# Optimization experiments

Hardware: AMD Instinct MI355X
Metric: run time of the kernel (lower is better)

Reference implementation:

```python
import jax, jax.numpy as jnp
import numpy as np

N_NODES = 50000


def _sage_conv(x, src, dst, W_l, b_l, W_r):
    # PyG SAGEConv (mean aggr): out = lin_l(mean_{j in N(i)} x_j) + lin_r(x_i)
    E = src.shape[0]
    msgs = x[src]                                            # [E, F] gather
    agg = jax.ops.segment_sum(msgs, dst, num_segments=N_NODES)
    deg = jax.ops.segment_sum(jnp.ones((E,), x.dtype), dst, num_segments=N_NODES)
    mean = agg / jnp.maximum(deg, 1.0)[:, None]              # zero-neighbor nodes stay 0
    return mean @ W_l.T + b_l + x @ W_r.T


def setup_inputs() -> dict:
    key = jax.random.key(0)
    k = jax.random.split(key, 8)
    F_in, H1, H2 = 128, 256, 128  # num_features, 2*emb, emb
    E = 800000
    x = jax.random.normal(k[0], (N_NODES, F_in), dtype=jnp.float32)
    edge_index = jax.random.randint(k[1], (2, E), 0, N_NODES, dtype=jnp.int64)
    s1 = 1.0 / np.sqrt(F_in)
    s2 = 1.0 / np.sqrt(H1)
    W1_l = jax.random.uniform(k[2], (H1, F_in), jnp.float32, -s1, s1)
    b1_l = jax.random.uniform(k[3], (H1,), jnp.float32, -s1, s1)
    W1_r = jax.random.uniform(k[4], (H1, F_in), jnp.float32, -s1, s1)
    W2_l = jax.random.uniform(k[5], (H2, H1), jnp.float32, -s2, s2)
    b2_l = jax.random.uniform(k[6], (H2,), jnp.float32, -s2, s2)
    W2_r = jax.random.uniform(k[7], (H2, H1), jnp.float32, -s2, s2)
    return {"x": x, "edge_index": edge_index,
            "W1_l": W1_l, "b1_l": b1_l, "W1_r": W1_r,
            "W2_l": W2_l, "b2_l": b2_l, "W2_r": W2_r}


def reference(x, edge_index, W1_l, b1_l, W1_r, W2_l, b2_l, W2_r):
    src, dst = edge_index[0], edge_index[1]
    h = jax.nn.relu(_sage_conv(x, src, dst, W1_l, b1_l, W1_r))
    # F.dropout(training=self.training): identity at inference
    out = _sage_conv(h, src, dst, W2_l, b2_l, W2_r)
    return out
```

## Files before the change

### kernel.cpp

```cpp
#include <hip/hip_runtime.h>


typedef short bf16x8 __attribute__((ext_vector_type(8)));
typedef float f32x4  __attribute__((ext_vector_type(4)));

__device__ __forceinline__ unsigned f2bf(float f) {
    unsigned u = __float_as_uint(f);
    return (u + 0x7FFFu + ((u >> 16) & 1u)) >> 16;
}
__device__ __forceinline__ unsigned pack2(float a, float b) {
    return f2bf(a) | (f2bf(b) << 16);
}
__device__ __forceinline__ float2 bfunpack(unsigned u) {
    return make_float2(__uint_as_float(u << 16), __uint_as_float(u & 0xffff0000u));
}

__device__ __forceinline__ void scan256(const int* __restrict__ h,
                                        int* __restrict__ out, int tid) {
    if (tid < 64) {
        const int i4 = tid * 4;
        const int v0 = h[i4], v1 = h[i4 + 1], v2 = h[i4 + 2], v3 = h[i4 + 3];
        const int t = v0 + v1 + v2 + v3;
        int x = t;
        #pragma unroll
        for (int dd = 1; dd < 64; dd <<= 1) {
            const int y = __shfl_up(x, dd, 64);
            if (tid >= dd) x += y;
        }
        const int ex = x - t;
        out[i4] = ex; out[i4 + 1] = ex + v0;
        out[i4 + 2] = ex + v0 + v1; out[i4 + 3] = ex + v0 + v1 + v2;
    }
}

__global__ __launch_bounds__(256)
void prep_kernel(const float* __restrict__ x, short* __restrict__ x_bf, long nx,
                 const float* __restrict__ W0, const float* __restrict__ W1,
                 const float* __restrict__ W2, const float* __restrict__ W3,
                 short* __restrict__ wbuf, int wn,
                 const int* __restrict__ dst, int* __restrict__ hist, int E,
                 int nbF, int nbW) {
    const int bx = blockIdx.x, tid = threadIdx.x;
    if (bx < nbF) {
        const long i = ((long)bx * 256 + tid) * 8;
        if (i + 8 <= nx) {
            const float4 a = *(const float4*)(x + i);
            const float4 b = *(const float4*)(x + i + 4);
            *(uint4*)(x_bf + i) = make_uint4(pack2(a.x, a.y), pack2(a.z, a.w),
                                             pack2(b.x, b.y), pack2(b.z, b.w));
        }
    } else if (bx < nbF + nbW) {
        const int rel = bx - nbF;
        const int w = rel >> 7;
        const float* __restrict__ W = (w == 0) ? W0 : (w == 1) ? W1 : (w == 2) ? W2 : W3;
        short* hi = wbuf + (long)(2 * w) * wn;
        short* lo = hi + wn;
        const int i = (rel & 127) * 256 + tid;
        if (i < wn) {
            const float v = W[i];
            const unsigned h = f2bf(v);
            hi[i] = (short)h;
            lo[i] = (short)f2bf(v - __uint_as_float(h << 16));
        }
    } else {
        const int hb = bx - nbF - nbW;
        #pragma unroll
        for (int k = 0; k < 4; ++k) {
            const int i = hb * 1024 + k * 256 + tid;
            if (i < E) atomicAdd(&hist[dst[i]], 1);
        }
    }
}

__global__ __launch_bounds__(256)
void scan_reduce_kernel(const int* __restrict__ hist, int* __restrict__ bsum, int M) {
    const long base = (long)blockIdx.x * 2048 + (long)threadIdx.x * 8;
    int s = 0;
    #pragma unroll
    for (int i = 0; i < 8; ++i) { const long idx = base + i; if (idx < M) s += hist[idx]; }
    #pragma unroll
    for (int d = 32; d; d >>= 1) s += __shfl_down(s, d, 64);
    __shared__ int ws[4];
    const int lane = threadIdx.x & 63, wid = threadIdx.x >> 6;
    if (lane == 0) ws[wid] = s;
    __syncthreads();
    if (threadIdx.x == 0) bsum[blockIdx.x] = ws[0] + ws[1] + ws[2] + ws[3];
}

__global__ void scan_root_kernel(int* __restrict__ bsum, int NB) {
    const int lane = threadIdx.x;
    const int v = (lane < NB) ? bsum[lane] : 0;
    int x = v;
    #pragma unroll
    for (int d = 1; d < 64; d <<= 1) { const int y = __shfl_up(x, d, 64); if (lane >= d) x += y; }
    if (lane < NB) bsum[lane] = x - v;
}

__global__ __launch_bounds__(256)
void scan_apply_kernel(int* __restrict__ hist, const int* __restrict__ bsum,
                       int* __restrict__ offs, int* __restrict__ gcur, int M, int E) {
    const long base = (long)blockIdx.x * 2048 + (long)threadIdx.x * 8;
    int v[8];
    #pragma unroll
    for (int i = 0; i < 8; ++i) { const long idx = base + i; v[i] = (idx < M) ? hist[idx] : 0; }
    int tsum = 0;
    #pragma unroll
    for (int i = 0; i < 8; ++i) { const int t = v[i]; v[i] = tsum; tsum += t; }
    const int lane = threadIdx.x & 63, wid = threadIdx.x >> 6;
    int x = tsum;
    #pragma unroll
    for (int d = 1; d < 64; d <<= 1) { const int y = __shfl_up(x, d, 64); if (lane >= d) x += y; }
    __shared__ int ws[4];
    if (lane == 63) ws[wid] = x;
    __syncthreads();
    int woff = bsum[blockIdx.x];
    if (wid > 0) woff += ws[0];
    if (wid > 1) woff += ws[1];
    if (wid > 2) woff += ws[2];
    const int texcl = woff + x - tsum;
    #pragma unroll
    for (int i = 0; i < 8; ++i) {
        const long idx = base + i;
        if (idx < M) {
            const int o = texcl + v[i];
            offs[idx] = o;
            hist[idx] = 0;
            if ((idx & 255) == 0) gcur[idx >> 8] = o;
        }
    }
    if (blockIdx.x == 0 && threadIdx.x == 0) offs[M] = E;
}

__global__ __launch_bounds__(1024)
void msplit_kernel(const int* __restrict__ src, const int* __restrict__ dst,
                   int* __restrict__ gcur, uint2* __restrict__ staging, int E) {
    __shared__ int hist[256], scanex[256], gb[256];
    __shared__ uint2 pairs[4096];
    const int tid = threadIdx.x;
    const long base = (long)blockIdx.x * 4096;
    const int cnt = min(4096, (int)(E - base));
    if (tid < 256) hist[tid] = 0;
    __syncthreads();
    int d[4], s[4];
    #pragma unroll
    for (int k = 0; k < 4; ++k) {
        const int i = tid + k * 1024;
        if (i < cnt) {
            d[k] = dst[base + i]; s[k] = src[base + i];
            atomicAdd(&hist[d[k] >> 8], 1);
        }
    }
    __syncthreads();
    scan256(hist, scanex, tid);
    __syncthreads();
    if (tid < 256) {
        const int c = hist[tid];
        gb[tid] = c ? atomicAdd(&gcur[tid], c) : 0;
        hist[tid] = scanex[tid];
    }
    __syncthreads();
    #pragma unroll
    for (int k = 0; k < 4; ++k) {
        const int i = tid + k * 1024;
        if (i < cnt) {
            const int b = d[k] >> 8;
            const int pos = atomicAdd(&hist[b], 1);
            pairs[pos] = make_uint2((unsigned)s[k], (unsigned)d[k]);
        }
    }
    __syncthreads();
    #pragma unroll
    for (int k = 0; k < 4; ++k) {
        const int i = tid + k * 1024;
        if (i < cnt) {
            const uint2 pr = pairs[i];
            const int b = (int)(pr.y >> 8);
            staging[gb[b] + (i - scanex[b])] = pr;
        }
    }
}

__global__ __launch_bounds__(1024)
void bsort_kernel(const uint2* __restrict__ staging, const int* __restrict__ offs,
                  int* __restrict__ fb_cur, int* __restrict__ src_sorted, int M) {
    const int b = blockIdx.x;
    const int n0 = b * 256;
    const int n1 = min(n0 + 256, M);
    const int s0 = offs[n0], s1 = offs[n1];
    const int cnt = s1 - s0;
    const int tid = threadIdx.x;
    if (cnt > 8192) {
        for (int i = tid; i < cnt; i += 1024) {
            const uint2 pr = staging[s0 + i];
            const int pos = offs[pr.y] + atomicAdd(&fb_cur[pr.y], 1);
            src_sorted[pos] = (int)pr.x;
        }
        return;
    }
    __shared__ int hist[256], base2[256];
    __shared__ int lsrc[8192];
    if (tid < 256) hist[tid] = 0;
    __syncthreads();
    for (int i = tid; i < cnt; i += 1024)
        atomicAdd(&hist[staging[s0 + i].y & 255], 1);
    __syncthreads();
    scan256(hist, base2, tid);
    __syncthreads();
    if (tid < 256) hist[tid] = base2[tid];
    __syncthreads();
    for (int i = tid; i < cnt; i += 1024) {
        const uint2 pr = staging[s0 + i];
        const int pos = atomicAdd(&hist[pr.y & 255], 1);
        lsrc[pos] = (int)pr.x;
    }
    __syncthreads();
    for (int i = tid; i < cnt; i += 1024)
        src_sorted[s0 + i] = lsrc[i];
}

template<int F, bool BF16_OUT, bool ADD>
__global__ __launch_bounds__(256)
void agg_mean_kernel(const short* __restrict__ feat, const int* __restrict__ src_sorted,
                     const int* __restrict__ offs, void* __restrict__ outv, int M) {
    const int node = blockIdx.x * 4 + (threadIdx.x >> 6);
    if (node >= M) return;
    const int lane = threadIdx.x & 63;
    const int start = offs[node], end = offs[node + 1];
    const unsigned* fb = (const unsigned*)feat;
    float2 acc = make_float2(0.f, 0.f);
    for (int e0 = start; e0 < end; e0 += 64) {
        const int n = min(64, end - e0);
        const int sv = (e0 + lane < end) ? src_sorted[e0 + lane] : 0;
        int j = 0;
        for (; j + 4 <= n; j += 4) {
            const int s0 = __shfl(sv, j, 64),     s1 = __shfl(sv, j + 1, 64);
            const int s2 = __shfl(sv, j + 2, 64), s3 = __shfl(sv, j + 3, 64);
            const unsigned u0 = fb[(long)s0 * (F / 2) + lane];
            const unsigned u1 = fb[(long)s1 * (F / 2) + lane];
            const unsigned u2 = fb[(long)s2 * (F / 2) + lane];
            const unsigned u3 = fb[(long)s3 * (F / 2) + lane];
            const float2 v0 = bfunpack(u0), v1 = bfunpack(u1);
            const float2 v2 = bfunpack(u2), v3 = bfunpack(u3);
            acc.x += (v0.x + v1.x) + (v2.x + v3.x);
            acc.y += (v0.y + v1.y) + (v2.y + v3.y);
        }
        for (; j < n; ++j) {
            const int s = __shfl(sv, j, 64);
            const float2 v = bfunpack(fb[(long)s * (F / 2) + lane]);
            acc.x += v.x; acc.y += v.y;
        }
    }
    const float inv = (end > start) ? 1.0f / (float)(end - start) : 0.f;
    acc.x *= inv; acc.y *= inv;
    if (BF16_OUT) {
        ((unsigned*)outv)[(long)node * (F / 2) + lane] = pack2(acc.x, acc.y);
    } else if (ADD) {
        float2* op = reinterpret_cast<float2*>((float*)outv + (long)node * F + lane * 2);
        const float2 cur = *op;
        *op = make_float2(cur.x + acc.x, cur.y + acc.y);
    } else {
        *reinterpret_cast<float2*>((float*)outv + (long)node * F + lane * 2) = acc;
    }
}

template<int KP>
__device__ __forceinline__ void gemm_phase(const short* __restrict__ A,
    const short* __restrict__ Whi, const short* __restrict__ Wlo,
    int M, int row0, int col0,
    short (*As)[40], short (*Bh)[40], short (*Bl)[40], f32x4 (&acc)[4][4])
{
    const int tid = threadIdx.x;
    const int lane = tid & 63;
    const int wr = (tid >> 7) & 1, wc = (tid >> 6) & 1;
    const int l15 = lane & 15, l4 = lane >> 4;
    const int sr = tid >> 1;
    const int sk = (tid & 1) * 16;
    const int gr = row0 + sr;

    for (int k0 = 0; k0 < KP; k0 += 32) {
        {
            const short* ap = A + (long)gr * KP + k0 + sk;
            uint4 v0 = make_uint4(0, 0, 0, 0), v1 = make_uint4(0, 0, 0, 0);
            if (gr < M) { v0 = *(const uint4*)ap; v1 = *(const uint4*)(ap + 8); }
            *(uint4*)&As[sr][sk]     = v0;
            *(uint4*)&As[sr][sk + 8] = v1;
        }
        {
            const short* bh = Whi + (long)(col0 + sr) * KP + k0 + sk;
            const short* bl = Wlo + (long)(col0 + sr) * KP + k0 + sk;
            *(uint4*)&Bh[sr][sk]     = *(const uint4*)bh;
            *(uint4*)&Bh[sr][sk + 8] = *(const uint4*)(bh + 8);
            *(uint4*)&Bl[sr][sk]     = *(const uint4*)bl;
            *(uint4*)&Bl[sr][sk + 8] = *(const uint4*)(bl + 8);
        }
        __syncthreads();
        bf16x8 bhf[4], blf[4];
        #pragma unroll
        for (int n = 0; n < 4; ++n) {
            const int br = wc * 64 + n * 16 + l15;
            bhf[n] = *(const bf16x8*)&Bh[br][l4 * 8];
            blf[n] = *(const bf16x8*)&Bl[br][l4 * 8];
        }
        #pragma unroll
        for (int m = 0; m < 4; ++m) {
            const bf16x8 af = *(const bf16x8*)&As[wr * 64 + m * 16 + l15][l4 * 8];
            #pragma unroll
            for (int n = 0; n < 4; ++n) {
                acc[m][n] = __builtin_amdgcn_mfma_f32_16x16x32_bf16(af, bhf[n], acc[m][n], 0, 0, 0);
                acc[m][n] = __builtin_amdgcn_mfma_f32_16x16x32_bf16(af, blf[n], acc[m][n], 0, 0, 0);
            }
        }
        __syncthreads();
    }
}

template<int K1, int K2, int NOUT, bool TWO_PHASE,
         bool RELU, bool HAS_BIAS, bool OUT_BF16>
__global__ __launch_bounds__(256)
void mfma_gemm(const short* __restrict__ A1, const short* __restrict__ A2,
               const short* __restrict__ B1hi, const short* __restrict__ B1lo,
               const short* __restrict__ B2hi, const short* __restrict__ B2lo,
               const float* __restrict__ bias, void* __restrict__ Cv, int M)
{
    __shared__ __align__(16) short As[128][40];
    __shared__ __align__(16) short Bh[128][40];
    __shared__ __align__(16) short Bl[128][40];
    const int row0 = blockIdx.x * 128, col0 = blockIdx.y * 128;
    f32x4 acc[4][4] = {};

    if constexpr (TWO_PHASE)
        gemm_phase<K1>(A1, B1hi, B1lo, M, row0, col0, As, Bh, Bl, acc);
    gemm_phase<K2>(A2, B2hi, B2lo, M, row0, col0, As, Bh, Bl, acc);

    const int tid = threadIdx.x, lane = tid & 63;
    const int wr = (tid >> 7) & 1, wc = (tid >> 6) & 1;
    const int l15 = lane & 15, l4 = lane >> 4;
    float bv[4];
    #pragma unroll
    for (int n = 0; n < 4; ++n)
        bv[n] = HAS_BIAS ? bias[col0 + wc * 64 + n * 16 + l15] : 0.f;
    #pragma unroll
    for (int m = 0; m < 4; ++m) {
        #pragma unroll
        for (int i = 0; i < 4; ++i) {
            const int r = row0 + wr * 64 + m * 16 + l4 * 4 + i;
            if (r < M) {
                #pragma unroll
                for (int n = 0; n < 4; ++n) {
                    const int c = col0 + wc * 64 + n * 16 + l15;
                    float v = acc[m][n][i] + bv[n];
                    if (RELU) v = fmaxf(v, 0.f);
                    if (OUT_BF16) ((short*)Cv)[(long)r * NOUT + c] = (short)f2bf(v);
                    else          ((float*)Cv)[(long)r * NOUT + c] = v;
                }
            }
        }
    }
}

template<int K, int NOUT>
__global__ __launch_bounds__(256)
void mfma_gemm_dual(const short* __restrict__ A,
                    const short* __restrict__ Wahi, const short* __restrict__ Walo,
                    const short* __restrict__ Wbhi, const short* __restrict__ Wblo,
                    const float* __restrict__ bias, short* __restrict__ Ca,
                    float* __restrict__ Cb, int M)
{
    __shared__ __align__(16) short As[128][40];
    __shared__ __align__(16) short Bh[2][128][40];
    __shared__ __align__(16) short Bl[2][128][40];
    const int row0 = blockIdx.x * 128;
    f32x4 acc[2][4][4] = {};

    const int tid = threadIdx.x, lane = tid & 63;
    const int wr = (tid >> 7) & 1, wc = (tid >> 6) & 1;
    const int l15 = lane & 15, l4 = lane >> 4;
    const int sr = tid >> 1;
    const int sk = (tid & 1) * 16;
    const int gr = row0 + sr;

    for (int k0 = 0; k0 < K; k0 += 32) {
        {
            const short* ap = A + (long)gr * K + k0 + sk;
            uint4 v0 = make_uint4(0, 0, 0, 0), v1 = make_uint4(0, 0, 0, 0);
            if (gr < M) { v0 = *(const uint4*)ap; v1 = *(const uint4*)(ap + 8); }
            *(uint4*)&As[sr][sk]     = v0;
            *(uint4*)&As[sr][sk + 8] = v1;
        }
        {
            const short* bh0 = Wahi + (long)sr * K + k0 + sk;
            const short* bl0 = Walo + (long)sr * K + k0 + sk;
            const short* bh1 = Wbhi + (long)sr * K + k0 + sk;
            const short* bl1 = Wblo + (long)sr * K + k0 + sk;
            *(uint4*)&Bh[0][sr][sk]     = *(const uint4*)bh0;
            *(uint4*)&Bh[0][sr][sk + 8] = *(const uint4*)(bh0 + 8);
            *(uint4*)&Bl[0][sr][sk]     = *(const uint4*)bl0;
            *(uint4*)&Bl[0][sr][sk + 8] = *(const uint4*)(bl0 + 8);
            *(uint4*)&Bh[1][sr][sk]     = *(const uint4*)bh1;
            *(uint4*)&Bh[1][sr][sk + 8] = *(const uint4*)(bh1 + 8);
            *(uint4*)&Bl[1][sr][sk]     = *(const uint4*)bl1;
            *(uint4*)&Bl[1][sr][sk + 8] = *(const uint4*)(bl1 + 8);
        }
        __syncthreads();
        bf16x8 af[4];
        #pragma unroll
        for (int m = 0; m < 4; ++m)
            af[m] = *(const bf16x8*)&As[wr * 64 + m * 16 + l15][l4 * 8];
        #pragma unroll
        for (int w = 0; w < 2; ++w) {
            #pragma unroll
            for (int n = 0; n < 4; ++n) {
                const int br = wc * 64 + n * 16 + l15;
                const bf16x8 bhf = *(const bf16x8*)&Bh[w][br][l4 * 8];
                const bf16x8 blf = *(const bf16x8*)&Bl[w][br][l4 * 8];
                #pragma unroll
                for (int m = 0; m < 4; ++m) {
                    acc[w][m][n] = __builtin_amdgcn_mfma_f32_16x16x32_bf16(af[m], bhf, acc[w][m][n], 0, 0, 0);
                    acc[w][m][n] = __builtin_amdgcn_mfma_f32_16x16x32_bf16(af[m], blf, acc[w][m][n], 0, 0, 0);
                }
            }
        }
        __syncthreads();
    }

    float bv[4];
    #pragma unroll
    for (int n = 0; n < 4; ++n)
        bv[n] = bias[wc * 64 + n * 16 + l15];
    #pragma unroll
    for (int m = 0; m < 4; ++m) {
        #pragma unroll
        for (int i = 0; i < 4; ++i) {
            const int r = row0 + wr * 64 + m * 16 + l4 * 4 + i;
            if (r < M) {
                #pragma unroll
                for (int n = 0; n < 4; ++n) {
                    const int c = wc * 64 + n * 16 + l15;
                    Ca[(long)r * NOUT + c] = (short)f2bf(acc[0][m][n][i]);
                    Cb[(long)r * NOUT + c] = acc[1][m][n][i] + bv[n];
                }
            }
        }
    }
}

extern "C" void kernel_launch(void* const* d_in, const int* in_sizes, int n_in,
                              void* d_out, int out_size, void* d_ws, size_t ws_size,
                              hipStream_t stream) {
    const float* x   = (const float*)d_in[0];
    const int*   ei  = (const int*)d_in[1];
    const float* W1l = (const float*)d_in[2];
    const float* b1  = (const float*)d_in[3];
    const float* W1r = (const float*)d_in[4];
    const float* W2l = (const float*)d_in[5];
    const float* b2  = (const float*)d_in[6];
    const float* W2r = (const float*)d_in[7];
    float* out = (float*)d_out;

    const int M = in_sizes[0] / 128;
    const int E = in_sizes[1] / 2;
    const int* src = ei;
    const int* dst = ei + E;

    const int Mal = ((M + 64 + 63) / 64) * 64;
    int* hist       = (int*)d_ws;
    int* offs       = hist + Mal;
    int* bsum       = offs + Mal;
    int* gcur       = bsum + 64;
    uint2* staging  = (uint2*)(gcur + 256);
    int* src_sorted = (int*)(staging + E);
    short* mean1_bf = (short*)(src_sorted + ((E + 63) / 64) * 64);
    short* p_bf     = mean1_bf + (long)M * 128;
    short* h_bf     = p_bf + (long)M * 128;
    short* wbuf     = h_bf + (long)M * 256;
    const int WN = 256 * 128;
    short *W1l_hi = wbuf,          *W1l_lo = wbuf + WN;
    short *W1r_hi = wbuf + 2 * WN, *W1r_lo = wbuf + 3 * WN;
    short *W2l_hi = wbuf + 4 * WN, *W2l_lo = wbuf + 5 * WN;
    short *W2r_hi = wbuf + 6 * WN, *W2r_lo = wbuf + 7 * WN;
    short* x_bf     = wbuf + 8 * WN;

    const int TB = 256;
    const int NB   = (M + 2047) / 2048;
    const int nbF  = (int)((long)M * 128 / 8 / TB);
    const int nbW  = 512;
    const int nbH  = (E + 1023) / 1024;
    const int NMS  = (E + 4095) / 4096;
    const int NBK  = (M + 255) / 256;

    hipMemsetAsync(hist, 0, (size_t)Mal * sizeof(int), stream);
    prep_kernel<<<dim3(nbF + nbW + nbH), dim3(TB), 0, stream>>>(
        x, x_bf, (long)M * 128, W1l, W1r, W2l, W2r, wbuf, WN, dst, hist, E, nbF, nbW);
    scan_reduce_kernel<<<dim3(NB), dim3(TB), 0, stream>>>(hist, bsum, M);
    scan_root_kernel<<<dim3(1), dim3(64), 0, stream>>>(bsum, NB);
    scan_apply_kernel<<<dim3(NB), dim3(TB), 0, stream>>>(hist, bsum, offs, gcur, M, E);
    msplit_kernel<<<dim3(NMS), dim3(1024), 0, stream>>>(src, dst, gcur, staging, E);
    bsort_kernel<<<dim3(NBK), dim3(1024), 0, stream>>>(staging, offs, hist, src_sorted, M);

    const int MB = (M + 127) / 128;

    agg_mean_kernel<128, true, false><<<dim3((M + 3) / 4), dim3(TB), 0, stream>>>(x_bf, src_sorted, offs, mean1_bf, M);
    mfma_gemm<128, 128, 256, true, true, true, true>
        <<<dim3(MB, 2), dim3(TB), 0, stream>>>(mean1_bf, x_bf, W1l_hi, W1l_lo, W1r_hi, W1r_lo,
                                               b1, h_bf, M);
    mfma_gemm_dual<256, 128>
        <<<dim3(MB), dim3(TB), 0, stream>>>(h_bf, W2l_hi, W2l_lo, W2r_hi, W2r_lo,
                                            b2, p_bf, out, M);
    agg_mean_kernel<128, false, true><<<dim3((M + 3) / 4), dim3(TB), 0, stream>>>(p_bf, src_sorted, offs, out, M);
}
```

Measured before the change: 278.5 us.

## Replace per-node histogram and three-pass scan with coarse bucket counts

```diff
diff --git a/kernel.cpp b/kernel.cpp
--- a/kernel.cpp
+++ b/kernel.cpp
@@ -38,8 +38,9 @@
                  const float* __restrict__ W0, const float* __restrict__ W1,
                  const float* __restrict__ W2, const float* __restrict__ W3,
                  short* __restrict__ wbuf, int wn,
-                 const int* __restrict__ dst, int* __restrict__ hist, int E,
+                 const int* __restrict__ dst, int* __restrict__ ccount, int E,
                  int nbF, int nbW) {
+    __shared__ int ch[256];
     const int bx = blockIdx.x, tid = threadIdx.x;
     if (bx < nbF) {
         const long i = ((long)bx * 256 + tid) * 8;
@@ -64,71 +65,44 @@
         }
     } else {
         const int hb = bx - nbF - nbW;
-        #pragma unroll
-        for (int k = 0; k < 4; ++k) {
-            const int i = hb * 1024 + k * 256 + tid;
-            if (i < E) atomicAdd(&hist[dst[i]], 1);
-        }
-    }
-}
-
-__global__ __launch_bounds__(256)
-void scan_reduce_kernel(const int* __restrict__ hist, int* __restrict__ bsum, int M) {
-    const long base = (long)blockIdx.x * 2048 + (long)threadIdx.x * 8;
-    int s = 0;
-    #pragma unroll
-    for (int i = 0; i < 8; ++i) { const long idx = base + i; if (idx < M) s += hist[idx]; }
-    #pragma unroll
-    for (int d = 32; d; d >>= 1) s += __shfl_down(s, d, 64);
-    __shared__ int ws[4];
-    const int lane = threadIdx.x & 63, wid = threadIdx.x >> 6;
-    if (lane == 0) ws[wid] = s;
-    __syncthreads();
-    if (threadIdx.x == 0) bsum[blockIdx.x] = ws[0] + ws[1] + ws[2] + ws[3];
-}
-
-__global__ void scan_root_kernel(int* __restrict__ bsum, int NB) {
+        ch[tid] = 0;
+        __syncthreads();
+        const long base = (long)hb * 8192;
+        #pragma unroll
+        for (int k = 0; k < 32; ++k) {
+            const long i = base + (long)k * 256 + tid;
+            if (i < E) atomicAdd(&ch[dst[i] >> 8], 1);
+        }
+        __syncthreads();
+        const int c = ch[tid];
+        if (c) atomicAdd(&ccount[tid], c);
+    }
+}
+
+__global__ void ccscan_kernel(const int* __restrict__ ccount, int* __restrict__ cbase,
+                              int* __restrict__ gcur, int NBK, int E) {
     const int lane = threadIdx.x;
-    const int v = (lane < NB) ? bsum[lane] : 0;
-    int x = v;
-    #pragma unroll
-    for (int d = 1; d < 64; d <<= 1) { const int y = __shfl_up(x, d, 64); if (lane >= d) x += y; }
-    if (lane < NB) bsum[lane] = x - v;
-}
-
-__global__ __launch_bounds__(256)
-void scan_apply_kernel(int* __restrict__ hist, const int* __restrict__ bsum,
-                       int* __restrict__ offs, int* __restrict__ gcur, int M, int E) {
-    const long base = (long)blockIdx.x * 2048 + (long)threadIdx.x * 8;
-    int v[8];
-    #pragma unroll
-    for (int i = 0; i < 8; ++i) { const long idx = base + i; v[i] = (idx < M) ? hist[idx] : 0; }
-    int tsum = 0;
-    #pragma unroll
-    for (int i = 0; i < 8; ++i) { const int t = v[i]; v[i] = tsum; tsum += t; }
-    const int lane = threadIdx.x & 63, wid = threadIdx.x >> 6;
-    int x = tsum;
-    #pragma unroll
-    for (int d = 1; d < 64; d <<= 1) { const int y = __shfl_up(x, d, 64); if (lane >= d) x += y; }
-    __shared__ int ws[4];
-    if (lane == 63) ws[wid] = x;
-    __syncthreads();
-    int woff = bsum[blockIdx.x];
-    if (wid > 0) woff += ws[0];
-    if (wid > 1) woff += ws[1];
-    if (wid > 2) woff += ws[2];
-    const int texcl = woff + x - tsum;
-    #pragma unroll
-    for (int i = 0; i < 8; ++i) {
-        const long idx = base + i;
-        if (idx < M) {
-            const int o = texcl + v[i];
-            offs[idx] = o;
-            hist[idx] = 0;
-            if ((idx & 255) == 0) gcur[idx >> 8] = o;
-        }
-    }
-    if (blockIdx.x == 0 && threadIdx.x == 0) offs[M] = E;
+    int v[4]; int t = 0;
+    #pragma unroll
+    for (int i = 0; i < 4; ++i) {
+        const int b = lane * 4 + i;
+        v[i] = (b < NBK) ? ccount[b] : 0;
+        t += v[i];
+    }
+    int x = t;
+    #pragma unroll
+    for (int d = 1; d < 64; d <<= 1) {
+        const int y = __shfl_up(x, d, 64);
+        if (lane >= d) x += y;
+    }
+    int ex = x - t;
+    #pragma unroll
+    for (int i = 0; i < 4; ++i) {
+        const int b = lane * 4 + i;
+        if (b < NBK) { cbase[b] = ex; gcur[b] = ex; }
+        ex += v[i];
+    }
+    if (lane == 63) cbase[NBK] = E;
 }
 
 __global__ __launch_bounds__(1024)
@@ -181,22 +155,14 @@
 }
 
 __global__ __launch_bounds__(1024)
-void bsort_kernel(const uint2* __restrict__ staging, const int* __restrict__ offs,
-                  int* __restrict__ fb_cur, int* __restrict__ src_sorted, int M) {
+void bsort_kernel(const uint2* __restrict__ staging, const int* __restrict__ cbase,
+                  int* __restrict__ offs, int* __restrict__ src_sorted,
+                  int M, int NBK) {
     const int b = blockIdx.x;
     const int n0 = b * 256;
-    const int n1 = min(n0 + 256, M);
-    const int s0 = offs[n0], s1 = offs[n1];
+    const int s0 = cbase[b], s1 = cbase[b + 1];
     const int cnt = s1 - s0;
     const int tid = threadIdx.x;
-    if (cnt > 8192) {
-        for (int i = tid; i < cnt; i += 1024) {
-            const uint2 pr = staging[s0 + i];
-            const int pos = offs[pr.y] + atomicAdd(&fb_cur[pr.y], 1);
-            src_sorted[pos] = (int)pr.x;
-        }
-        return;
-    }
     __shared__ int hist[256], base2[256];
     __shared__ int lsrc[8192];
     if (tid < 256) hist[tid] = 0;
@@ -206,16 +172,29 @@
     __syncthreads();
     scan256(hist, base2, tid);
     __syncthreads();
-    if (tid < 256) hist[tid] = base2[tid];
-    __syncthreads();
-    for (int i = tid; i < cnt; i += 1024) {
-        const uint2 pr = staging[s0 + i];
-        const int pos = atomicAdd(&hist[pr.y & 255], 1);
-        lsrc[pos] = (int)pr.x;
-    }
-    __syncthreads();
-    for (int i = tid; i < cnt; i += 1024)
-        src_sorted[s0 + i] = lsrc[i];
+    if (tid < 256) {
+        const int node = n0 + tid;
+        if (node < M) offs[node] = s0 + base2[tid];
+        hist[tid] = base2[tid];
+    }
+    if (b == NBK - 1 && tid == 0) offs[M] = s1;
+    __syncthreads();
+    if (cnt <= 8192) {
+        for (int i = tid; i < cnt; i += 1024) {
+            const uint2 pr = staging[s0 + i];
+            const int pos = atomicAdd(&hist[pr.y & 255], 1);
+            lsrc[pos] = (int)pr.x;
+        }
+        __syncthreads();
+        for (int i = tid; i < cnt; i += 1024)
+            src_sorted[s0 + i] = lsrc[i];
+    } else {
+        for (int i = tid; i < cnt; i += 1024) {
+            const uint2 pr = staging[s0 + i];
+            const int pos = atomicAdd(&hist[pr.y & 255], 1);
+            src_sorted[s0 + pos] = (int)pr.x;
+        }
+    }
 }
 
 template<int F, bool BF16_OUT, bool ADD>
@@ -462,12 +441,14 @@
     const int* src = ei;
     const int* dst = ei + E;
 
-    const int Mal = ((M + 64 + 63) / 64) * 64;
-    int* hist       = (int*)d_ws;
-    int* offs       = hist + Mal;
-    int* bsum       = offs + Mal;
-    int* gcur       = bsum + 64;
-    uint2* staging  = (uint2*)(gcur + 256);
+    const int NBK = (M + 255) / 256;
+    const int Mal = ((M + 1 + 63) / 64) * 64;
+
+    int* ccount     = (int*)d_ws;
+    int* cbase      = ccount + 256;
+    int* gcur       = cbase + 320;
+    int* offs       = gcur + 256;
+    uint2* staging  = (uint2*)(offs + Mal);
     int* src_sorted = (int*)(staging + E);
     short* mean1_bf = (short*)(src_sorted + ((E + 63) / 64) * 64);
     short* p_bf     = mean1_bf + (long)M * 128;
@@ -481,21 +462,17 @@
     short* x_bf     = wbuf + 8 * WN;
 
     const int TB = 256;
-    const int NB   = (M + 2047) / 2048;
-    const int nbF  = (int)((long)M * 128 / 8 / TB);
+    const int nbF  = (int)(((long)M * 128 / 8 + TB - 1) / TB);
     const int nbW  = 512;
-    const int nbH  = (E + 1023) / 1024;
+    const int nbC  = (E + 8191) / 8192;
     const int NMS  = (E + 4095) / 4096;
-    const int NBK  = (M + 255) / 256;
-
-    hipMemsetAsync(hist, 0, (size_t)Mal * sizeof(int), stream);
-    prep_kernel<<<dim3(nbF + nbW + nbH), dim3(TB), 0, stream>>>(
-        x, x_bf, (long)M * 128, W1l, W1r, W2l, W2r, wbuf, WN, dst, hist, E, nbF, nbW);
-    scan_reduce_kernel<<<dim3(NB), dim3(TB), 0, stream>>>(hist, bsum, M);
-    scan_root_kernel<<<dim3(1), dim3(64), 0, stream>>>(bsum, NB);
-    scan_apply_kernel<<<dim3(NB), dim3(TB), 0, stream>>>(hist, bsum, offs, gcur, M, E);
+
+    hipMemsetAsync(ccount, 0, 256 * sizeof(int), stream);
+    prep_kernel<<<dim3(nbF + nbW + nbC), dim3(TB), 0, stream>>>(
+        x, x_bf, (long)M * 128, W1l, W1r, W2l, W2r, wbuf, WN, dst, ccount, E, nbF, nbW);
+    ccscan_kernel<<<dim3(1), dim3(64), 0, stream>>>(ccount, cbase, gcur, NBK, E);
     msplit_kernel<<<dim3(NMS), dim3(1024), 0, stream>>>(src, dst, gcur, staging, E);
-    bsort_kernel<<<dim3(NBK), dim3(1024), 0, stream>>>(staging, offs, hist, src_sorted, M);
+    bsort_kernel<<<dim3(NBK), dim3(1024), 0, stream>>>(staging, cbase, offs, src_sorted, M, NBK);
 
     const int MB = (M + 127) / 128;
 
```

New measurement: 243.8 us, median of 2. 12.4% less time.
